# Kernel optimization log

Hardware: AMD Instinct MI355X
Metric: run time of the kernel (lower is better)

## Reference

```python
import jax, jax.numpy as jnp
import numpy as np

T, H, I, E, TOP_K = 4096, 2048, 1024, 16, 2
I_SHARED = 1024  # moe_intermediate_size * n_shared_experts


def _silu_and_mul(gu):
    g, u = jnp.split(gu, 2, axis=-1)
    return jax.nn.silu(g) * u


def setup_inputs() -> dict:
    key = jax.random.key(0)
    ks = jax.random.split(key, 8)
    s = 0.02
    return {
        "hidden_states": jax.random.normal(ks[0], (T, H), jnp.float32),
        "gate_w": jax.random.normal(ks[1], (E, H), jnp.float32) * s,          # router
        "w1": jax.random.normal(ks[2], (E, 2 * I, H), jnp.float32) * s,       # expert gate_up
        "b1": jax.random.normal(ks[3], (E, 2 * I), jnp.float32) * s,
        "w2": jax.random.normal(ks[4], (E, H, I), jnp.float32) * s,           # expert down
        "sg_w": jax.random.normal(ks[5], (2 * I_SHARED, H), jnp.float32) * s, # shared gate_up
        "sg_b": jax.random.normal(ks[6], (2 * I_SHARED,), jnp.float32) * s,
        "sd_w": jax.random.normal(ks[7], (H, I_SHARED), jnp.float32) * s,     # shared down
    }


def reference(hidden_states, gate_w, w1, b1, w2, sg_w, sg_b, sd_w):
    x = hidden_states  # [T, H]

    # shared expert MLP (gate_up has bias, down does not)
    shared = _silu_and_mul(x @ sg_w.T + sg_b) @ sd_w.T  # [T, H]

    # router: softmax -> top-k -> renormalize (norm_topk_prob=True)
    probs = jax.nn.softmax(x @ gate_w.T, axis=-1)       # [T, E]
    wts, idx = jax.lax.top_k(probs, TOP_K)              # [T, k]
    wts = wts / jnp.sum(wts, axis=-1, keepdims=True)

    # per-expert combine coefficient: coef[e, t] = sum_k wts[t,k] * (idx[t,k]==e)
    coef = jnp.sum(jax.nn.one_hot(idx, E, dtype=x.dtype) * wts[..., None], axis=1).T  # [E, T]

    def body(acc, params):
        w1e, b1e, w2e, ce = params
        a = _silu_and_mul(x @ w1e.T + b1e)   # [T, I]
        return acc + ce[:, None] * (a @ w2e.T), None

    out, _ = jax.lax.scan(body, jnp.zeros_like(x), (w1, b1, w2, coef))
    return out + shared
```

## Files before the change

kernel.cpp:

```cpp
#include <hip/hip_runtime.h>
#include <hip/hip_bf16.h>
#include <stdint.h>

#define T_TOK 4096
#define H_DIM 2048
#define I_DIM 1024
#define NEXP  16
#define NROWS 16384

typedef short bf16x8 __attribute__((ext_vector_type(8)));
typedef float f32x4  __attribute__((ext_vector_type(4)));
typedef unsigned short u16;

__device__ __forceinline__ u16 f2b(float f) {
  union { __hip_bfloat16 h; u16 u; } cv;
  cv.h = __float2bfloat16(f);
  return cv.u;
}

__device__ __forceinline__ void gload16(const void* g, void* l) {
  __builtin_amdgcn_global_load_lds((const __attribute__((address_space(1))) void*)g,
                                   (__attribute__((address_space(3))) void*)l, 16, 0, 0);
}

__global__ __launch_bounds__(256) void cvt4_kernel(const float4* __restrict__ src,
                                                   ushort4* __restrict__ dst, int n4) {
  int i = blockIdx.x * 256 + threadIdx.x;
  int stride = gridDim.x * 256;
  for (; i < n4; i += stride) {
    float4 v = src[i];
    ushort4 o;
    o.x = f2b(v.x); o.y = f2b(v.y); o.z = f2b(v.z); o.w = f2b(v.w);
    dst[i] = o;
  }
}

__global__ __launch_bounds__(256) void router_kernel(const float* __restrict__ x,
                                                     const float* __restrict__ gw,
                                                     int* __restrict__ sel,
                                                     float* __restrict__ selw,
                                                     int* __restrict__ counts) {
  int t = blockIdx.x;
  int tid = threadIdx.x;
  const float* xr = x + (size_t)t * H_DIM;
  double p[NEXP];
#pragma unroll
  for (int e = 0; e < NEXP; ++e) p[e] = 0.0;
#pragma unroll
  for (int j = 0; j < 8; ++j) {
    int h = tid * 8 + j;
    double xv = (double)xr[h];
#pragma unroll
    for (int e = 0; e < NEXP; ++e) p[e] += xv * (double)gw[e * H_DIM + h];
  }
#pragma unroll
  for (int e = 0; e < NEXP; ++e) {
#pragma unroll
    for (int off = 32; off > 0; off >>= 1) p[e] += __shfl_down(p[e], off);
  }
  __shared__ double sm[4][NEXP];
  int w = tid >> 6;
  if ((tid & 63) == 0) {
#pragma unroll
    for (int e = 0; e < NEXP; ++e) sm[w][e] = p[e];
  }
  __syncthreads();
  if (tid == 0) {
    double l0 = -1e300, l1 = -1e300;
    int e0 = 0, e1 = 0;
    for (int e = 0; e < NEXP; ++e) {
      double v = sm[0][e] + sm[1][e] + sm[2][e] + sm[3][e];
      if (v > l0) { l1 = l0; e1 = e0; l0 = v; e0 = e; }
      else if (v > l1) { l1 = v; e1 = e; }
    }
    double w0 = 1.0 / (1.0 + exp(l1 - l0));
    sel[t * 2 + 0] = e0;
    sel[t * 2 + 1] = e1;
    selw[t * 2 + 0] = (float)w0;
    selw[t * 2 + 1] = (float)(1.0 - w0);
    atomicAdd(&counts[e0], 1);
    atomicAdd(&counts[e1], 1);
  }
}

__global__ void prefix_kernel(const int* __restrict__ counts, int* __restrict__ rowbase) {
  if (threadIdx.x == 0 && blockIdx.x == 0) {
    int acc = 0;
    for (int e = 0; e < NEXP; ++e) {
      rowbase[e] = acc;
      acc += (counts[e] + 255) & ~255;
    }
    rowbase[NEXP] = acc;
  }
}

__global__ __launch_bounds__(256) void scatter_kernel(const int* __restrict__ sel,
                                                      const float* __restrict__ selw,
                                                      const int* __restrict__ rowbase,
                                                      int* __restrict__ cursor,
                                                      int* __restrict__ tok_of_row,
                                                      float* __restrict__ coef_of_row) {
  int idx = blockIdx.x * 256 + threadIdx.x;
  if (idx < T_TOK * 2) {
    int t = idx >> 1;
    int e = sel[idx];
    int slot = atomicAdd(&cursor[e], 1);
    int row = rowbase[e] + slot;
    tok_of_row[row] = t;
    coef_of_row[row] = selw[idx];
  } else if (idx < T_TOK * 3) {
    int t = idx - T_TOK * 2;
    int sb = rowbase[NEXP];
    tok_of_row[sb + t] = t;
    coef_of_row[sb + t] = 1.0f;
  }
}


__global__ __launch_bounds__(256, 4) void gemm1_kernel(
    const u16* __restrict__ x_bf, const u16* __restrict__ W1cat,
    const float* __restrict__ b1, const float* __restrict__ sg_b,
    const int* __restrict__ tok_of_row, const int* __restrict__ counts,
    const int* __restrict__ rowbase, u16* __restrict__ abuf) {
  int nt = blockIdx.x, rt = blockIdx.y, e = blockIdx.z;
  int n_e = (e < NEXP) ? counts[e] : T_TOK;
  if (rt * 128 >= n_e) return;
  int rbase = rowbase[e];
  int n_valid = n_e - rt * 128;
  if (n_valid > 128) n_valid = 128;

  __shared__ short As[128 * 64];
  __shared__ short Bs[128 * 64];
  __shared__ int Ts[128];

  int tid = threadIdx.x;
  if (tid < 128) Ts[tid] = tok_of_row[rbase + rt * 128 + tid];
  __syncthreads();

  int wavebase = tid & 0xC0;
  const u16* srcA[4];
  short* dstA[4];
  const u16* srcB[4];
  short* dstB[4];
#pragma unroll
  for (int p = 0; p < 4; ++p) {
    int c = p * 256 + tid;
    int r = c >> 3;
    int koff = ((c & 7) * 8) ^ ((r & 7) << 3);
    int tok = Ts[r]; if (tok < 0) tok = 0;
    srcA[p] = x_bf + (size_t)tok * H_DIM + koff;
    dstA[p] = &As[(p * 256 + wavebase) * 8];
    int gr = (r & 1) ? (I_DIM + nt * 64 + (r >> 1)) : (nt * 64 + (r >> 1));
    srcB[p] = W1cat + ((size_t)e * (2 * I_DIM) + gr) * H_DIM + koff;
    dstB[p] = &Bs[(p * 256 + wavebase) * 8];
  }

  f32x4 acc[4][4];
#pragma unroll
  for (int m = 0; m < 4; ++m)
#pragma unroll
    for (int n = 0; n < 4; ++n) acc[m][n] = (f32x4){0.f, 0.f, 0.f, 0.f};

  int lane = tid & 63, w = tid >> 6, wr = w >> 1, wc = w & 1;
  int laneq = lane & 15, hi = lane >> 4;

  for (int kt = 0; kt < H_DIM / 64; ++kt) {
    if (kt) __syncthreads();
#pragma unroll
    for (int p = 0; p < 4; ++p) gload16(srcA[p] + kt * 64, dstA[p]);
#pragma unroll
    for (int p = 0; p < 4; ++p) gload16(srcB[p] + kt * 64, dstB[p]);
    __syncthreads();
#pragma unroll
    for (int ks = 0; ks < 2; ++ks) {
      bf16x8 a[4], b[4];
#pragma unroll
      for (int f = 0; f < 4; ++f) {
        int rowA = wr * 64 + f * 16 + laneq;
        int rowB = wc * 64 + f * 16 + laneq;
        a[f] = *(const bf16x8*)(As + rowA * 64 + ((ks * 32 + hi * 8) ^ ((rowA & 7) << 3)));
        b[f] = *(const bf16x8*)(Bs + rowB * 64 + ((ks * 32 + hi * 8) ^ ((rowB & 7) << 3)));
      }
#pragma unroll
      for (int f = 0; f < 4; ++f)
#pragma unroll
        for (int fn = 0; fn < 4; ++fn)
          acc[f][fn] = __builtin_amdgcn_mfma_f32_16x16x32_bf16(a[f], b[fn], acc[f][fn], 0, 0, 0);
    }
  }

  const float* bias = (e < NEXP) ? (b1 + (size_t)e * (2 * I_DIM)) : sg_b;
  bool evenl = !(lane & 1);
  float bs[4];
#pragma unroll
  for (int nf = 0; nf < 4; ++nf) {
    int j = (wc * 64 + nf * 16 + laneq) >> 1;
    bs[nf] = evenl ? bias[nt * 64 + j] : bias[I_DIM + nt * 64 + j];
  }
#pragma unroll
  for (int mf = 0; mf < 4; ++mf) {
#pragma unroll
    for (int nf = 0; nf < 4; ++nf) {
      int j = (wc * 64 + nf * 16 + laneq) >> 1;
#pragma unroll
      for (int reg = 0; reg < 4; ++reg) {
        int r = wr * 64 + mf * 16 + hi * 4 + reg;
        float v = acc[mf][nf][reg] + bs[nf];
        float o = __shfl_xor(v, 1);
        if (evenl && r < n_valid) {
          float g = v, u = o;
          float s = g / (1.0f + __expf(-g));
          abuf[(size_t)(rbase + rt * 128 + r) * I_DIM + nt * 64 + j] = f2b(s * u);
        }
      }
    }
  }
}

template <int ATOMIC>
__global__ __launch_bounds__(256, 4) void gemm2_kernel(
    const u16* __restrict__ abuf, const u16* __restrict__ W2cat,
    const int* __restrict__ tok_of_row, const float* __restrict__ coef_of_row,
    const int* __restrict__ counts, const int* __restrict__ rowbase,
    float* __restrict__ out, int e_force) {
  int nt = blockIdx.x, rt = blockIdx.y;
  int e = (e_force >= 0) ? e_force : (int)blockIdx.z;
  int n_e = (e < NEXP) ? counts[e] : T_TOK;
  if (rt * 128 >= n_e) return;
  int rbase = rowbase[e];
  int n_valid = n_e - rt * 128;
  if (n_valid > 128) n_valid = 128;

  __shared__ short As[128 * 64];
  __shared__ short Bs[128 * 64];
  __shared__ int Ts[128];
  __shared__ float Cs[128];

  int tid = threadIdx.x;
  if (tid < 128) {
    int row = rbase + rt * 128 + tid;
    Ts[tid] = tok_of_row[row];
    Cs[tid] = coef_of_row[row];
  }
  __syncthreads();

  int wavebase = tid & 0xC0;
  const u16* srcA[4];
  short* dstA[4];
  const u16* srcB[4];
  short* dstB[4];
#pragma unroll
  for (int p = 0; p < 4; ++p) {
    int c = p * 256 + tid;
    int r = c >> 3;
    int koff = ((c & 7) * 8) ^ ((r & 7) << 3);
    srcA[p] = abuf + (size_t)(rbase + rt * 128 + r) * I_DIM + koff;
    dstA[p] = &As[(p * 256 + wavebase) * 8];
    srcB[p] = W2cat + ((size_t)e * H_DIM + nt * 128 + r) * I_DIM + koff;
    dstB[p] = &Bs[(p * 256 + wavebase) * 8];
  }

  f32x4 acc[4][4];
#pragma unroll
  for (int m = 0; m < 4; ++m)
#pragma unroll
    for (int n = 0; n < 4; ++n) acc[m][n] = (f32x4){0.f, 0.f, 0.f, 0.f};

  int lane = tid & 63, w = tid >> 6, wr = w >> 1, wc = w & 1;
  int laneq = lane & 15, hi = lane >> 4;

  for (int kt = 0; kt < I_DIM / 64; ++kt) {
    if (kt) __syncthreads();
#pragma unroll
    for (int p = 0; p < 4; ++p) gload16(srcA[p] + kt * 64, dstA[p]);
#pragma unroll
    for (int p = 0; p < 4; ++p) gload16(srcB[p] + kt * 64, dstB[p]);
    __syncthreads();
#pragma unroll
    for (int ks = 0; ks < 2; ++ks) {
      bf16x8 a[4], b[4];
#pragma unroll
      for (int f = 0; f < 4; ++f) {
        int rowA = wr * 64 + f * 16 + laneq;
        int rowB = wc * 64 + f * 16 + laneq;
        a[f] = *(const bf16x8*)(As + rowA * 64 + ((ks * 32 + hi * 8) ^ ((rowA & 7) << 3)));
        b[f] = *(const bf16x8*)(Bs + rowB * 64 + ((ks * 32 + hi * 8) ^ ((rowB & 7) << 3)));
      }
#pragma unroll
      for (int f = 0; f < 4; ++f)
#pragma unroll
        for (int fn = 0; fn < 4; ++fn)
          acc[f][fn] = __builtin_amdgcn_mfma_f32_16x16x32_bf16(a[f], b[fn], acc[f][fn], 0, 0, 0);
    }
  }

#pragma unroll
  for (int mf = 0; mf < 4; ++mf) {
#pragma unroll
    for (int nf = 0; nf < 4; ++nf) {
      int col = nt * 128 + wc * 64 + nf * 16 + laneq;
#pragma unroll
      for (int reg = 0; reg < 4; ++reg) {
        int r = wr * 64 + mf * 16 + hi * 4 + reg;
        if (r < n_valid) {
          int tok = Ts[r];
          float val = acc[mf][nf][reg] * Cs[r];
          float* p = out + (size_t)tok * H_DIM + col;
          if (ATOMIC) atomicAdd(p, val);
          else *p = val;
        }
      }
    }
  }
}

extern "C" void kernel_launch(void* const* d_in, const int* in_sizes, int n_in,
                              void* d_out, int out_size, void* d_ws, size_t ws_size,
                              hipStream_t stream) {
  const float* x    = (const float*)d_in[0];
  const float* gate_w = (const float*)d_in[1];
  const float* w1   = (const float*)d_in[2];
  const float* b1   = (const float*)d_in[3];
  const float* w2   = (const float*)d_in[4];
  const float* sg_w = (const float*)d_in[5];
  const float* sg_b = (const float*)d_in[6];
  const float* sd_w = (const float*)d_in[7];
  float* out = (float*)d_out;

  uint8_t* ws = (uint8_t*)d_ws;
  size_t off = 0;
  auto alloc = [&](size_t bytes) -> void* {
    void* p = ws + off;
    off += (bytes + 255) & ~(size_t)255;
    return p;
  };
  u16*  W1cat = (u16*)alloc((size_t)17 * 2048 * 2048 * 2);
  u16*  W2cat = (u16*)alloc((size_t)17 * 2048 * 1024 * 2);
  u16*  x_bf  = (u16*)alloc((size_t)T_TOK * H_DIM * 2);
  u16*  abuf  = (u16*)alloc((size_t)NROWS * I_DIM * 2);
  int*  tok_of_row  = (int*)alloc((size_t)NROWS * 4);
  float* coef_of_row = (float*)alloc((size_t)NROWS * 4);
  int*  sel   = (int*)alloc((size_t)T_TOK * 2 * 4);
  float* selw = (float*)alloc((size_t)T_TOK * 2 * 4);
  int*  counts  = (int*)alloc(256);
  int*  cursor  = (int*)alloc(256);
  int*  rowbase = (int*)alloc(256);
  (void)ws_size; (void)in_sizes; (void)n_in; (void)out_size;

  hipMemsetAsync(counts, 0, 768, stream);
  hipMemsetAsync(tok_of_row, 0xFF, (size_t)NROWS * 4, stream);

  auto cvt = [&](const float* s, u16* d, size_t n) {
    int n4 = (int)(n / 4);
    int blocks = (n4 + 255) / 256;
    if (blocks > 2048) blocks = 2048;
    cvt4_kernel<<<dim3(blocks), dim3(256), 0, stream>>>((const float4*)s, (ushort4*)d, n4);
  };
  cvt(w1,   W1cat, (size_t)16 * 2048 * 2048);
  cvt(sg_w, W1cat + (size_t)16 * 2048 * 2048, (size_t)2048 * 2048);
  cvt(w2,   W2cat, (size_t)16 * 2048 * 1024);
  cvt(sd_w, W2cat + (size_t)16 * 2048 * 1024, (size_t)2048 * 1024);
  cvt(x,    x_bf, (size_t)T_TOK * H_DIM);

  router_kernel<<<dim3(T_TOK), dim3(256), 0, stream>>>(x, gate_w, sel, selw, counts);
  prefix_kernel<<<dim3(1), dim3(64), 0, stream>>>(counts, rowbase);
  scatter_kernel<<<dim3(48), dim3(256), 0, stream>>>(sel, selw, rowbase, cursor, tok_of_row, coef_of_row);

  gemm1_kernel<<<dim3(16, 32, 17), dim3(256), 0, stream>>>(
      x_bf, W1cat, b1, sg_b, tok_of_row, counts, rowbase, abuf);

  gemm2_kernel<0><<<dim3(16, 32, 1), dim3(256), 0, stream>>>(
      abuf, W2cat, tok_of_row, coef_of_row, counts, rowbase, out, NEXP);
  gemm2_kernel<1><<<dim3(16, 32, 16), dim3(256), 0, stream>>>(
      abuf, W2cat, tok_of_row, coef_of_row, counts, rowbase, out, -1);
}
```

Measured before the change: 540.8 us.

## Fuse weight conversions, fold x cast into router, reorder gate/up tiles

Merges the four weight fp32-to-bf16 conversion launches into one kernel and moves the activation cast into the router kernel, which already reads x. Expert row padding shrinks from 256 to 128 rows, which cuts wasted padded rows. The gemm1 B tile now loads gate and up rows as two contiguous halves instead of interleaving them, so the SiLU*mul epilogue pairs accumulators inside each thread and drops the shuffle and the half-idle lanes. The cost is a branchy conversion loop and a different fragment mapping.

Result: faster. 523.9 us (-3.1%).

```diff
diff --git a/kernel.cpp b/kernel.cpp
--- a/kernel.cpp
+++ b/kernel.cpp
@@ -23,15 +23,27 @@
                                    (__attribute__((address_space(3))) void*)l, 16, 0, 0);
 }
 
-__global__ __launch_bounds__(256) void cvt4_kernel(const float4* __restrict__ src,
-                                                   ushort4* __restrict__ dst, int n4) {
+__global__ __launch_bounds__(256) void cvtall_kernel(
+    const float4* __restrict__ w1, const float4* __restrict__ sgw,
+    const float4* __restrict__ w2, const float4* __restrict__ sdw,
+    ushort4* __restrict__ W1cat, ushort4* __restrict__ W2cat) {
+  const int N0 = 16 * 2048 * 2048 / 4;
+  const int N1 = 2048 * 2048 / 4;
+  const int N2 = 16 * 2048 * 1024 / 4;
+  const int N3 = 2048 * 1024 / 4;
+  const int total = N0 + N1 + N2 + N3;
   int i = blockIdx.x * 256 + threadIdx.x;
   int stride = gridDim.x * 256;
-  for (; i < n4; i += stride) {
-    float4 v = src[i];
+  for (; i < total; i += stride) {
+    const float4* s; ushort4* d; int k;
+    if (i < N0)            { s = w1;  d = W1cat;      k = i; }
+    else if (i < N0 + N1)  { s = sgw; d = W1cat + N0; k = i - N0; }
+    else if (i < N0 + N1 + N2) { s = w2; d = W2cat;   k = i - N0 - N1; }
+    else                   { s = sdw; d = W2cat + N2; k = i - N0 - N1 - N2; }
+    float4 v = s[k];
     ushort4 o;
     o.x = f2b(v.x); o.y = f2b(v.y); o.z = f2b(v.z); o.w = f2b(v.w);
-    dst[i] = o;
+    d[k] = o;
   }
 }
 
@@ -39,20 +51,25 @@
                                                      const float* __restrict__ gw,
                                                      int* __restrict__ sel,
                                                      float* __restrict__ selw,
-                                                     int* __restrict__ counts) {
+                                                     int* __restrict__ counts,
+                                                     u16* __restrict__ x_bf) {
   int t = blockIdx.x;
   int tid = threadIdx.x;
   const float* xr = x + (size_t)t * H_DIM;
   double p[NEXP];
 #pragma unroll
   for (int e = 0; e < NEXP; ++e) p[e] = 0.0;
+  bf16x8 xs;
 #pragma unroll
   for (int j = 0; j < 8; ++j) {
     int h = tid * 8 + j;
-    double xv = (double)xr[h];
+    float xf = xr[h];
+    xs[j] = (short)f2b(xf);
+    double xv = (double)xf;
 #pragma unroll
     for (int e = 0; e < NEXP; ++e) p[e] += xv * (double)gw[e * H_DIM + h];
   }
+  *(bf16x8*)(x_bf + (size_t)t * H_DIM + tid * 8) = xs;
 #pragma unroll
   for (int e = 0; e < NEXP; ++e) {
 #pragma unroll
@@ -88,7 +105,7 @@
     int acc = 0;
     for (int e = 0; e < NEXP; ++e) {
       rowbase[e] = acc;
-      acc += (counts[e] + 255) & ~255;
+      acc += (counts[e] + 127) & ~127;
     }
     rowbase[NEXP] = acc;
   }
@@ -150,7 +167,7 @@
     int tok = Ts[r]; if (tok < 0) tok = 0;
     srcA[p] = x_bf + (size_t)tok * H_DIM + koff;
     dstA[p] = &As[(p * 256 + wavebase) * 8];
-    int gr = (r & 1) ? (I_DIM + nt * 64 + (r >> 1)) : (nt * 64 + (r >> 1));
+    int gr = (r < 64) ? (nt * 64 + r) : (I_DIM + nt * 64 + (r - 64));
     srcB[p] = W1cat + ((size_t)e * (2 * I_DIM) + gr) * H_DIM + koff;
     dstB[p] = &Bs[(p * 256 + wavebase) * 8];
   }
@@ -177,8 +194,8 @@
 #pragma unroll
       for (int f = 0; f < 4; ++f) {
         int rowA = wr * 64 + f * 16 + laneq;
-        int rowB = wc * 64 + f * 16 + laneq;
         a[f] = *(const bf16x8*)(As + rowA * 64 + ((ks * 32 + hi * 8) ^ ((rowA & 7) << 3)));
+        int rowB = ((f < 2) ? (wc * 32 + f * 16) : (64 + wc * 32 + (f - 2) * 16)) + laneq;
         b[f] = *(const bf16x8*)(Bs + rowB * 64 + ((ks * 32 + hi * 8) ^ ((rowB & 7) << 3)));
       }
 #pragma unroll
@@ -190,27 +207,21 @@
   }
 
   const float* bias = (e < NEXP) ? (b1 + (size_t)e * (2 * I_DIM)) : sg_b;
-  bool evenl = !(lane & 1);
-  float bs[4];
-#pragma unroll
-  for (int nf = 0; nf < 4; ++nf) {
-    int j = (wc * 64 + nf * 16 + laneq) >> 1;
-    bs[nf] = evenl ? bias[nt * 64 + j] : bias[I_DIM + nt * 64 + j];
-  }
-#pragma unroll
-  for (int mf = 0; mf < 4; ++mf) {
-#pragma unroll
-    for (int nf = 0; nf < 4; ++nf) {
-      int j = (wc * 64 + nf * 16 + laneq) >> 1;
+#pragma unroll
+  for (int nf = 0; nf < 2; ++nf) {
+    int j = nt * 64 + wc * 32 + nf * 16 + laneq;
+    float bg = bias[j];
+    float bu = bias[I_DIM + j];
+#pragma unroll
+    for (int mf = 0; mf < 4; ++mf) {
 #pragma unroll
       for (int reg = 0; reg < 4; ++reg) {
         int r = wr * 64 + mf * 16 + hi * 4 + reg;
-        float v = acc[mf][nf][reg] + bs[nf];
-        float o = __shfl_xor(v, 1);
-        if (evenl && r < n_valid) {
-          float g = v, u = o;
+        if (r < n_valid) {
+          float g = acc[mf][nf][reg] + bg;
+          float u = acc[mf][nf + 2][reg] + bu;
           float s = g / (1.0f + __expf(-g));
-          abuf[(size_t)(rbase + rt * 128 + r) * I_DIM + nt * 64 + j] = f2b(s * u);
+          abuf[(size_t)(rbase + rt * 128 + r) * I_DIM + j] = f2b(s * u);
         }
       }
     }
@@ -350,19 +361,11 @@
   hipMemsetAsync(counts, 0, 768, stream);
   hipMemsetAsync(tok_of_row, 0xFF, (size_t)NROWS * 4, stream);
 
-  auto cvt = [&](const float* s, u16* d, size_t n) {
-    int n4 = (int)(n / 4);
-    int blocks = (n4 + 255) / 256;
-    if (blocks > 2048) blocks = 2048;
-    cvt4_kernel<<<dim3(blocks), dim3(256), 0, stream>>>((const float4*)s, (ushort4*)d, n4);
-  };
-  cvt(w1,   W1cat, (size_t)16 * 2048 * 2048);
-  cvt(sg_w, W1cat + (size_t)16 * 2048 * 2048, (size_t)2048 * 2048);
-  cvt(w2,   W2cat, (size_t)16 * 2048 * 1024);
-  cvt(sd_w, W2cat + (size_t)16 * 2048 * 1024, (size_t)2048 * 1024);
-  cvt(x,    x_bf, (size_t)T_TOK * H_DIM);
-
-  router_kernel<<<dim3(T_TOK), dim3(256), 0, stream>>>(x, gate_w, sel, selw, counts);
+  cvtall_kernel<<<dim3(3072), dim3(256), 0, stream>>>(
+      (const float4*)w1, (const float4*)sg_w, (const float4*)w2, (const float4*)sd_w,
+      (ushort4*)W1cat, (ushort4*)W2cat);
+
+  router_kernel<<<dim3(T_TOK), dim3(256), 0, stream>>>(x, gate_w, sel, selw, counts, x_bf);
   prefix_kernel<<<dim3(1), dim3(64), 0, stream>>>(counts, rowbase);
   scatter_kernel<<<dim3(48), dim3(256), 0, stream>>>(sel, selw, rowbase, cursor, tok_of_row, coef_of_row);
 
```
